# Optimization experiments

Hardware: AMD Instinct MI355X
Metric: run time of the kernel (lower is better)

The kernel has to match this reference:

```python
import jax, jax.numpy as jnp
import numpy as np

L = 4          # encoder layers
D = 1280       # d_model
H = 20         # heads
DH = D // H
FF = 5120
MEL = 128
S = 1500       # post-conv seq len
EPS = 1e-6


def quant_per_token(x):
    # dynamic per-token int8 quant: scale = max|x|/127
    s = jnp.max(jnp.abs(x), axis=-1, keepdims=True) / 127.0
    s = jnp.maximum(s, 1e-8)
    q = jnp.clip(jnp.round(x / s), -128, 127)
    return q, s


def w8a8_linear(qx, sx, w, b):
    # per-output-channel int8 weight quant, W8A8 GEMM, fp dequant epilogue
    ws = jnp.maximum(jnp.max(jnp.abs(w), axis=1, keepdims=True) / 127.0, 1e-8)  # [O,1]
    qw = jnp.clip(jnp.round(w / ws), -128, 127)
    y = qx @ qw.T                        # int-valued accum in fp32
    return y * sx * ws[:, 0][None, :] + b[None, :]


def rmsnorm_quant(x, w, b):
    # rms_norm_general: w * x / sqrt(E[x^2]+eps) + b, then per-token quant
    inv = jax.lax.rsqrt(jnp.mean(x * x, axis=-1, keepdims=True) + EPS)
    return quant_per_token(x * inv * w[None, :] + b[None, :])


def conv1d(x, w, b, stride, pad):
    y = jax.lax.conv_general_dilated(x, w, (stride,), [(pad, pad)],
                                     dimension_numbers=('NCW', 'OIW', 'NCW'))
    return y + b[None, :, None]


def setup_inputs() -> dict:
    key = jax.random.key(0)
    ks = jax.random.split(key, 24)
    n = lambda k, sh, sc=0.02: jax.random.normal(k, sh, jnp.float32) * sc
    return {
        'input_features': jax.random.normal(ks[0], (1, MEL, 2 * S), jnp.float32),
        'conv1_w': n(ks[1], (D, MEL, 3)), 'conv1_b': n(ks[2], (D,)),
        'conv2_w': n(ks[3], (D, D, 3)), 'conv2_b': n(ks[4], (D,)),
        'pos_emb': n(ks[5], (S, D)),
        'ln1_w': jnp.ones((L, D)), 'ln1_b': n(ks[6], (L, D)),
        'qkv_w': n(ks[7], (L, 3 * D, D)), 'qkv_b': n(ks[8], (L, 3 * D)),
        'out_w': n(ks[9], (L, D, D)), 'out_b': n(ks[10], (L, D)),
        'ln2_w': jnp.ones((L, D)), 'ln2_b': n(ks[11], (L, D)),
        'fc1_w': n(ks[12], (L, FF, D)), 'fc1_b': n(ks[13], (L, FF)),
        'fc2_w': n(ks[14], (L, D, FF)), 'fc2_b': n(ks[15], (L, D)),
        'lnf_w': jnp.ones((D,)), 'lnf_b': n(ks[16], (D,)),
    }


def reference(input_features, conv1_w, conv1_b, conv2_w, conv2_b, pos_emb,
              ln1_w, ln1_b, qkv_w, qkv_b, out_w, out_b,
              ln2_w, ln2_b, fc1_w, fc1_b, fc2_w, fc2_b, lnf_w, lnf_b):
    B = input_features.shape[0]
    h = jax.nn.gelu(conv1d(input_features, conv1_w, conv1_b, 1, 1))
    h = jax.nn.gelu(conv1d(h, conv2_w, conv2_b, 2, 1))
    h = h.transpose(0, 2, 1) + pos_emb[None]          # [B,S,D]
    h = h.reshape(B * S, D)
    scale = DH ** -0.5
    for l in range(L):
        res = h
        qx, sx = rmsnorm_quant(h, ln1_w[l], ln1_b[l])
        qkv = w8a8_linear(qx, sx, qkv_w[l], qkv_b[l])  # [B*S, 3D]
        q, k, v = jnp.split(qkv.reshape(B, S, 3, H, DH), 3, axis=2)
        q, k, v = q[:, :, 0], k[:, :, 0], v[:, :, 0]   # [B,S,H,DH]
        scores = jnp.einsum('bqhd,bkhd->bhqk', q, k) * scale
        attn = jax.nn.softmax(scores, axis=-1)
        ao = jnp.einsum('bhqk,bkhd->bqhd', attn, v).reshape(B * S, D)
        qa, sa = quant_per_token(ao)
        h = res + w8a8_linear(qa, sa, out_w[l], out_b[l])
        res = h
        qx, sx = rmsnorm_quant(h, ln2_w[l], ln2_b[l])
        f1 = w8a8_linear(qx, sx, fc1_w[l], fc1_b[l])
        qm, sm = quant_per_token(jax.nn.gelu(f1))
        h = res + w8a8_linear(qm, sm, fc2_w[l], fc2_b[l])
    h = h.reshape(B, S, D)
    # avg_pooler: AvgPool1d(kernel=2, stride=2) over time
    h = h.reshape(B, S // 2, 2, D).mean(axis=2)
    # final LayerNorm (true layernorm, fp path)
    mu = jnp.mean(h, axis=-1, keepdims=True)
    var = jnp.mean(jnp.square(h - mu), axis=-1, keepdims=True)
    h = (h - mu) * jax.lax.rsqrt(var + 1e-5) * lnf_w + lnf_b
    return h
```

## Files before the change

### kernel.cpp

```cpp
#include <hip/hip_runtime.h>
#include <stdint.h>

#define S_LEN 1500
#define D_MODEL 1280
#define N_HEAD 20
#define D_HEAD 64
#define FF_DIM 5120
#define N_LAYER 4

typedef int v4i __attribute__((ext_vector_type(4)));
typedef short v8s __attribute__((ext_vector_type(8)));
typedef float v4f __attribute__((ext_vector_type(4)));


__device__ inline float gelu_tanh(float x) {
    float x3 = x * x * x;
    return 0.5f * x * (1.0f + tanhf(0.7978845608028654f * (x + 0.044715f * x3)));
}

__device__ inline float wred_sum(float v) {
    for (int o = 32; o > 0; o >>= 1) v += __shfl_down(v, o, 64);
    return v;
}
__device__ inline float wred_max(float v) {
    for (int o = 32; o > 0; o >>= 1) v = fmaxf(v, __shfl_down(v, o, 64));
    return v;
}
__device__ inline float block_sum(float v, float* sm4) {
    v = wred_sum(v);
    int w = threadIdx.x >> 6;
    if ((threadIdx.x & 63) == 0) sm4[w] = v;
    __syncthreads();
    float r = sm4[0] + sm4[1] + sm4[2] + sm4[3];
    __syncthreads();
    return r;
}
__device__ inline float block_max(float v, float* sm4) {
    v = wred_max(v);
    int w = threadIdx.x >> 6;
    if ((threadIdx.x & 63) == 0) sm4[w] = v;
    __syncthreads();
    float r = fmaxf(fmaxf(sm4[0], sm4[1]), fmaxf(sm4[2], sm4[3]));
    __syncthreads();
    return r;
}

__device__ inline unsigned short f2bf(float x) {
    unsigned int u = __float_as_uint(x);
    u += 0x7fffu + ((u >> 16) & 1u);
    return (unsigned short)(u >> 16);
}
__device__ inline float bf2f(unsigned short h) {
    return __uint_as_float(((unsigned int)h) << 16);
}

__device__ inline void gload_lds16(const void* g, void* l) {
    __builtin_amdgcn_global_load_lds(
        (const __attribute__((address_space(1))) char*)g,
        (__attribute__((address_space(3))) char*)l, 16, 0, 0);
}


__global__ __launch_bounds__(256) void im2col1_kernel(
    const float* __restrict__ x, unsigned short* __restrict__ Ah,
    unsigned short* __restrict__ Al)
{
    int t = blockIdx.x * 256 + threadIdx.x;
    int col = blockIdx.y;
    if (t >= 3000) return;
    int tap = col >> 7, i = col & 127;
    int src = t - 1 + tap;
    float v = (src >= 0 && src < 3000) ? x[(size_t)i * 3000 + src] : 0.0f;
    unsigned short h = f2bf(v);
    Ah[(size_t)t * 384 + col] = h;
    Al[(size_t)t * 384 + col] = f2bf(v - bf2f(h));
}

__global__ __launch_bounds__(256) void im2col2_kernel(
    const float* __restrict__ g1, unsigned short* __restrict__ Ah,
    unsigned short* __restrict__ Al)
{
    int col = blockIdx.x * 256 + threadIdx.x;
    int t = blockIdx.y;
    if (col >= 3840) return;
    int tap = col / 1280, o = col - tap * 1280;
    int src = 2 * t - 1 + tap;
    float v = (src >= 0 && src < 3000) ? g1[(size_t)src * 1280 + o] : 0.0f;
    unsigned short h = f2bf(v);
    Ah[(size_t)t * 3840 + col] = h;
    Al[(size_t)t * 3840 + col] = f2bf(v - bf2f(h));
}

__global__ __launch_bounds__(256) void wreorder_kernel(
    const float* __restrict__ w, unsigned short* __restrict__ woh,
    unsigned short* __restrict__ wol, int C)
{
    int o = blockIdx.x;
    int KC = 3 * C;
    const float* wr = w + (size_t)o * KC;
    for (int col = threadIdx.x; col < KC; col += 256) {
        int tap = col / C, i = col - tap * C;
        float v = wr[i * 3 + tap];
        unsigned short h = f2bf(v);
        woh[(size_t)o * KC + col] = h;
        wol[(size_t)o * KC + col] = f2bf(v - bf2f(h));
    }
}

template <int EPI>
__global__ __launch_bounds__(256, 2) void gemm_conv_bf16x3(
    const unsigned short* __restrict__ Ah, const unsigned short* __restrict__ Al,
    const unsigned short* __restrict__ Wh, const unsigned short* __restrict__ Wl,
    const float* __restrict__ bias, const float* __restrict__ pos,
    float* __restrict__ out, int M, int N, int K, int nTilesN)
{
    __shared__ unsigned short lds[2][4][128][32];
    int tid = threadIdx.x;
    int lane = tid & 63;
    int wv = tid >> 6;
    int l15 = lane & 15, quad = lane >> 4;
    int wm = wv >> 1, wn = wv & 1;

    int nwg = gridDim.x;
    int cpx = nwg >> 3;
    int bid = blockIdx.x;
    int swz = (bid & 7) * cpx + (bid >> 3);
    int bx = swz % nTilesN, by = swz / nTilesN;
    int m0 = by * 128, n0 = bx * 128;

    const unsigned short* splane = (wv == 0) ? Ah : (wv == 1) ? Al : (wv == 2) ? Wh : Wl;
    int rbase = (wv < 2) ? m0 : n0;
    int rlim  = (wv < 2) ? M : N;
    const unsigned short* srcp[8];
    #pragma unroll
    for (int c = 0; c < 8; c++) {
        int row = rbase + c * 16 + (lane >> 2);
        if (row >= rlim) row = rlim - 1;
        srcp[c] = splane + (size_t)row * K + (lane & 3) * 8;
    }

    auto stage = [&](int nb, int k0) {
        char* lbase = (char*)&lds[nb][wv][0][0];
        #pragma unroll
        for (int c = 0; c < 8; c++)
            gload_lds16(srcp[c] + k0, lbase + c * 1024);
    };

    v4f acc[4][4];
    #pragma unroll
    for (int i = 0; i < 4; i++)
        #pragma unroll
        for (int j = 0; j < 4; j++) acc[i][j] = (v4f){0.0f, 0.0f, 0.0f, 0.0f};

    int nsteps = K >> 5;
    stage(0, 0);
    __syncthreads();
    int cur = 0;
    for (int t = 0; t < nsteps; t++) {
        if (t + 1 < nsteps) stage(cur ^ 1, (t + 1) * 32);
        v8s ah[4], al2[4], bh[4], bl[4];
        #pragma unroll
        for (int i = 0; i < 4; i++) {
            ah[i]  = *(const v8s*)&lds[cur][0][wm * 64 + i * 16 + l15][quad * 8];
            al2[i] = *(const v8s*)&lds[cur][1][wm * 64 + i * 16 + l15][quad * 8];
            bh[i]  = *(const v8s*)&lds[cur][2][wn * 64 + i * 16 + l15][quad * 8];
            bl[i]  = *(const v8s*)&lds[cur][3][wn * 64 + i * 16 + l15][quad * 8];
        }
        #pragma unroll
        for (int i = 0; i < 4; i++)
            #pragma unroll
            for (int j = 0; j < 4; j++) {
                acc[i][j] = __builtin_amdgcn_mfma_f32_16x16x32_bf16(ah[i],  bh[j], acc[i][j], 0, 0, 0);
                acc[i][j] = __builtin_amdgcn_mfma_f32_16x16x32_bf16(al2[i], bh[j], acc[i][j], 0, 0, 0);
                acc[i][j] = __builtin_amdgcn_mfma_f32_16x16x32_bf16(ah[i],  bl[j], acc[i][j], 0, 0, 0);
            }
        __syncthreads();
        cur ^= 1;
    }

    #pragma unroll
    for (int i = 0; i < 4; i++) {
        #pragma unroll
        for (int j = 0; j < 4; j++) {
            int n = n0 + wn * 64 + j * 16 + l15;
            float bn = bias[n];
            #pragma unroll
            for (int r = 0; r < 4; r++) {
                int m = m0 + wm * 64 + i * 16 + quad * 4 + r;
                if (m < M) {
                    float v = gelu_tanh(acc[i][j][r] + bn);
                    if (EPI == 1) v += pos[(size_t)m * N + n];
                    out[(size_t)m * N + n] = v;
                }
            }
        }
    }
}


__global__ __launch_bounds__(256) void wquant_kernel(
    const float* __restrict__ w, int8_t* __restrict__ qw,
    float* __restrict__ ws, int K)
{
    int r = blockIdx.x;
    int tid = threadIdx.x;
    __shared__ float sm4[4];
    const float4* wr = (const float4*)(w + (size_t)r * K);
    int n4 = K >> 2;
    float mx = 0.0f;
    for (int i = tid; i < n4; i += 256) {
        float4 v = wr[i];
        mx = fmaxf(mx, fmaxf(fmaxf(fabsf(v.x), fabsf(v.y)), fmaxf(fabsf(v.z), fabsf(v.w))));
    }
    mx = block_max(mx, sm4);
    float sc = fmaxf(mx / 127.0f, 1e-8f);
    if (tid == 0) ws[r] = sc;
    float rs = 1.0f / sc;
    char4* qr = (char4*)(qw + (size_t)r * K);
    for (int i = tid; i < n4; i += 256) {
        float4 v = wr[i];
        char4 q;
        q.x = (int8_t)fminf(fmaxf(rintf(v.x * rs), -128.0f), 127.0f);
        q.y = (int8_t)fminf(fmaxf(rintf(v.y * rs), -128.0f), 127.0f);
        q.z = (int8_t)fminf(fmaxf(rintf(v.z * rs), -128.0f), 127.0f);
        q.w = (int8_t)fminf(fmaxf(rintf(v.w * rs), -128.0f), 127.0f);
        qr[i] = q;
    }
}

__global__ __launch_bounds__(256) void rmsnorm_quant_kernel(
    const float* __restrict__ x, const float* __restrict__ w,
    const float* __restrict__ b, int8_t* __restrict__ q,
    float* __restrict__ sx)
{
    int s = blockIdx.x;
    int tid = threadIdx.x;
    __shared__ float sm4[4];
    const float* xr = x + (size_t)s * D_MODEL;
    float v[5];
    float ss = 0.0f;
    for (int i = 0; i < 5; i++) {
        float t = xr[tid + 256 * i];
        v[i] = t;
        ss += t * t;
    }
    ss = block_sum(ss, sm4);
    float inv = rsqrtf(ss * (1.0f / 1280.0f) + 1e-6f);
    float mx = 0.0f;
    for (int i = 0; i < 5; i++) {
        int idx = tid + 256 * i;
        float t = v[i] * inv * w[idx] + b[idx];
        v[i] = t;
        mx = fmaxf(mx, fabsf(t));
    }
    mx = block_max(mx, sm4);
    float sc = fmaxf(mx / 127.0f, 1e-8f);
    if (tid == 0) sx[s] = sc;
    float rs = 1.0f / sc;
    for (int i = 0; i < 5; i++) {
        float qv = rintf(v[i] * rs);
        qv = fminf(fmaxf(qv, -128.0f), 127.0f);
        q[(size_t)s * D_MODEL + tid + 256 * i] = (int8_t)qv;
    }
}

template <bool GELU>
__global__ __launch_bounds__(256) void quant_kernel(
    const float* __restrict__ x, int8_t* __restrict__ q,
    float* __restrict__ sx, int Dm)
{
    int s = blockIdx.x;
    int tid = threadIdx.x;
    __shared__ float sm4[4];
    const float4* xr = (const float4*)(x + (size_t)s * Dm);
    int n4 = Dm >> 2;
    float mx = 0.0f;
    for (int i = tid; i < n4; i += 256) {
        float4 t = xr[i];
        if (GELU) { t.x = gelu_tanh(t.x); t.y = gelu_tanh(t.y); t.z = gelu_tanh(t.z); t.w = gelu_tanh(t.w); }
        mx = fmaxf(mx, fmaxf(fmaxf(fabsf(t.x), fabsf(t.y)), fmaxf(fabsf(t.z), fabsf(t.w))));
    }
    mx = block_max(mx, sm4);
    float sc = fmaxf(mx / 127.0f, 1e-8f);
    if (tid == 0) sx[s] = sc;
    float rs = 1.0f / sc;
    char4* qr = (char4*)(q + (size_t)s * Dm);
    for (int i = tid; i < n4; i += 256) {
        float4 t = xr[i];
        if (GELU) { t.x = gelu_tanh(t.x); t.y = gelu_tanh(t.y); t.z = gelu_tanh(t.z); t.w = gelu_tanh(t.w); }
        char4 qq;
        qq.x = (int8_t)fminf(fmaxf(rintf(t.x * rs), -128.0f), 127.0f);
        qq.y = (int8_t)fminf(fmaxf(rintf(t.y * rs), -128.0f), 127.0f);
        qq.z = (int8_t)fminf(fmaxf(rintf(t.z * rs), -128.0f), 127.0f);
        qq.w = (int8_t)fminf(fmaxf(rintf(t.w * rs), -128.0f), 127.0f);
        qr[i] = qq;
    }
}

__global__ __launch_bounds__(256) void gemm_w8a8_mfma(
    const int8_t* __restrict__ qx, const float* __restrict__ sx,
    const int8_t* __restrict__ qw, const float* __restrict__ ws,
    const float* __restrict__ bias, const float* __restrict__ res,
    float* __restrict__ out, int M, int O, int K)
{
    int lane = threadIdx.x & 63;
    int wv = threadIdx.x >> 6;
    int l15 = lane & 15;
    int quad = lane >> 4;
    int m_base = blockIdx.y * 64 + wv * 16;
    int n_base = blockIdx.x * 64;

    int ar = m_base + l15; if (ar >= M) ar = M - 1;
    const int8_t* ap = qx + (size_t)ar * K + quad * 16;
    const int8_t* bp = qw + (size_t)(n_base + l15) * K + quad * 16;
    size_t rowK16 = (size_t)16 * K;

    v4i acc0 = {0, 0, 0, 0}, acc1 = {0, 0, 0, 0}, acc2 = {0, 0, 0, 0}, acc3 = {0, 0, 0, 0};
    int nsteps = K >> 6;
    for (int s = 0; s < nsteps; s++) {
        v4i a  = *(const v4i*)(ap + s * 64);
        v4i b0 = *(const v4i*)(bp + s * 64);
        v4i b1 = *(const v4i*)(bp + rowK16 + s * 64);
        v4i b2 = *(const v4i*)(bp + 2 * rowK16 + s * 64);
        v4i b3 = *(const v4i*)(bp + 3 * rowK16 + s * 64);
        acc0 = __builtin_amdgcn_mfma_i32_16x16x64_i8(a, b0, acc0, 0, 0, 0);
        acc1 = __builtin_amdgcn_mfma_i32_16x16x64_i8(a, b1, acc1, 0, 0, 0);
        acc2 = __builtin_amdgcn_mfma_i32_16x16x64_i8(a, b2, acc2, 0, 0, 0);
        acc3 = __builtin_amdgcn_mfma_i32_16x16x64_i8(a, b3, acc3, 0, 0, 0);
    }

    float sxv[4];
    #pragma unroll
    for (int r = 0; r < 4; r++) {
        int m = m_base + quad * 4 + r;
        sxv[r] = (m < M) ? sx[m] : 0.0f;
    }
    v4i accs[4] = {acc0, acc1, acc2, acc3};
    #pragma unroll
    for (int nb = 0; nb < 4; nb++) {
        int n = n_base + nb * 16 + l15;
        float wn = ws[n];
        float bn = bias[n];
        #pragma unroll
        for (int r = 0; r < 4; r++) {
            int m = m_base + quad * 4 + r;
            if (m < M) {
                float y = (float)accs[nb][r] * sxv[r] * wn + bn;
                if (res) y += res[(size_t)m * O + n];
                out[(size_t)m * O + n] = y;
            }
        }
    }
}

__global__ __launch_bounds__(256) void attn_tiled_kernel(
    const float* __restrict__ qkv, float* __restrict__ ao)
{
    __shared__ float Qs[64][68];
    __shared__ float KV[64][68];
    __shared__ float Ps[64][68];
    int h = blockIdx.y;
    int q_tile = blockIdx.x;
    int tid = threadIdx.x;
    int tx = tid & 15, ty = tid >> 4;
    int q0 = ty * 4;
    int d0 = tx * 4;

    {
        int r = tid >> 2;
        int dq = (tid & 3) * 16;
        int qg = q_tile * 64 + r;
        int qc = qg < S_LEN ? qg : S_LEN - 1;
        const float4* src = (const float4*)(qkv + (size_t)qc * 3840 + h * 64 + dq);
        #pragma unroll
        for (int i = 0; i < 4; i++)
            *(float4*)&Qs[r][dq + i * 4] = src[i];
    }

    float O[4][4] = {};
    float m_run[4], l_run[4];
    #pragma unroll
    for (int i = 0; i < 4; i++) { m_run[i] = -INFINITY; l_run[i] = 0.0f; }

    for (int kt = 0; kt < 24; kt++) {
        int kbase = kt * 64;
        int krem = S_LEN - kbase;

        __syncthreads();
        {
            int kk = tid >> 2;
            int dq = (tid & 3) * 16;
            int kg = kbase + kk;
            int kc = kg < S_LEN ? kg : S_LEN - 1;
            const float4* src = (const float4*)(qkv + (size_t)kc * 3840 + 1280 + h * 64 + dq);
            #pragma unroll
            for (int i = 0; i < 4; i++) {
                float4 v = src[i];
                KV[dq + i * 4 + 0][kk] = v.x;
                KV[dq + i * 4 + 1][kk] = v.y;
                KV[dq + i * 4 + 2][kk] = v.z;
                KV[dq + i * 4 + 3][kk] = v.w;
            }
        }
        __syncthreads();

        float s[4][4] = {};
        int k0loc = tx * 4;
        for (int d = 0; d < 64; d += 4) {
            float4 qv[4], kv[4];
            #pragma unroll
            for (int i = 0; i < 4; i++) qv[i] = *(const float4*)&Qs[q0 + i][d];
            #pragma unroll
            for (int dd = 0; dd < 4; dd++) kv[dd] = *(const float4*)&KV[d + dd][k0loc];
            #pragma unroll
            for (int i = 0; i < 4; i++) {
                float qa[4] = {qv[i].x, qv[i].y, qv[i].z, qv[i].w};
                #pragma unroll
                for (int dd = 0; dd < 4; dd++) {
                    float kb[4] = {kv[dd].x, kv[dd].y, kv[dd].z, kv[dd].w};
                    #pragma unroll
                    for (int j = 0; j < 4; j++)
                        s[i][j] += qa[dd] * kb[j];
                }
            }
        }

        #pragma unroll
        for (int i = 0; i < 4; i++)
            #pragma unroll
            for (int j = 0; j < 4; j++) {
                s[i][j] *= 0.125f;
                if (k0loc + j >= krem) s[i][j] = -INFINITY;
            }

        #pragma unroll
        for (int i = 0; i < 4; i++) {
            float t = fmaxf(fmaxf(s[i][0], s[i][1]), fmaxf(s[i][2], s[i][3]));
            #pragma unroll
            for (int msk = 1; msk < 16; msk <<= 1)
                t = fmaxf(t, __shfl_xor(t, msk, 64));
            float mn = fmaxf(m_run[i], t);
            float alpha = __expf(m_run[i] - mn);
            m_run[i] = mn;
            float rs = 0.0f;
            #pragma unroll
            for (int j = 0; j < 4; j++) {
                float p = __expf(s[i][j] - mn);
                s[i][j] = p;
                rs += p;
            }
            #pragma unroll
            for (int msk = 1; msk < 16; msk <<= 1)
                rs += __shfl_xor(rs, msk, 64);
            l_run[i] = l_run[i] * alpha + rs;
            #pragma unroll
            for (int j = 0; j < 4; j++) O[i][j] *= alpha;
            *(float4*)&Ps[q0 + i][k0loc] = *(float4*)&s[i][0];
        }
        __syncthreads();

        {
            int kk = tid >> 2;
            int dq = (tid & 3) * 16;
            int kg = kbase + kk;
            int kc = kg < S_LEN ? kg : S_LEN - 1;
            const float4* src = (const float4*)(qkv + (size_t)kc * 3840 + 2560 + h * 64 + dq);
            #pragma unroll
            for (int i = 0; i < 4; i++)
                *(float4*)&KV[kk][dq + i * 4] = src[i];
        }
        __syncthreads();

        for (int kb = 0; kb < 64; kb += 4) {
            float4 pv[4], vv[4];
            #pragma unroll
            for (int i = 0; i < 4; i++) pv[i] = *(const float4*)&Ps[q0 + i][kb];
            #pragma unroll
            for (int kk = 0; kk < 4; kk++) vv[kk] = *(const float4*)&KV[kb + kk][d0];
            #pragma unroll
            for (int i = 0; i < 4; i++) {
                float pa[4] = {pv[i].x, pv[i].y, pv[i].z, pv[i].w};
                #pragma unroll
                for (int kk = 0; kk < 4; kk++) {
                    float vb[4] = {vv[kk].x, vv[kk].y, vv[kk].z, vv[kk].w};
                    #pragma unroll
                    for (int j = 0; j < 4; j++)
                        O[i][j] += pa[kk] * vb[j];
                }
            }
        }
    }

    #pragma unroll
    for (int i = 0; i < 4; i++) {
        int qg = q_tile * 64 + q0 + i;
        if (qg < S_LEN) {
            float rl = 1.0f / l_run[i];
            float4 o;
            o.x = O[i][0] * rl; o.y = O[i][1] * rl; o.z = O[i][2] * rl; o.w = O[i][3] * rl;
            *(float4*)(ao + (size_t)qg * D_MODEL + h * 64 + d0) = o;
        }
    }
}

__global__ __launch_bounds__(256) void pool_ln_kernel(
    const float* __restrict__ h, const float* __restrict__ w,
    const float* __restrict__ b, float* __restrict__ out)
{
    int t = blockIdx.x;
    int tid = threadIdx.x;
    __shared__ float sm4[4];
    const float* r0 = h + (size_t)(2 * t) * D_MODEL;
    const float* r1 = r0 + D_MODEL;
    float v[5];
    float s1 = 0.0f;
    for (int i = 0; i < 5; i++) {
        int idx = tid + 256 * i;
        float x = 0.5f * (r0[idx] + r1[idx]);
        v[i] = x;
        s1 += x;
    }
    float mu = block_sum(s1, sm4) * (1.0f / 1280.0f);
    float s2 = 0.0f;
    for (int i = 0; i < 5; i++) {
        float d = v[i] - mu;
        s2 += d * d;
    }
    float var = block_sum(s2, sm4) * (1.0f / 1280.0f);
    float inv = rsqrtf(var + 1e-5f);
    for (int i = 0; i < 5; i++) {
        int idx = tid + 256 * i;
        out[(size_t)t * D_MODEL + idx] = (v[i] - mu) * inv * w[idx] + b[idx];
    }
}


static inline size_t al256(size_t x) { return (x + 255) & ~(size_t)255; }

extern "C" void kernel_launch(void* const* d_in, const int* in_sizes, int n_in,
                              void* d_out, int out_size, void* d_ws, size_t ws_size,
                              hipStream_t stream) {
    const float* in_feat = (const float*)d_in[0];
    const float* conv1_w = (const float*)d_in[1];
    const float* conv1_b = (const float*)d_in[2];
    const float* conv2_w = (const float*)d_in[3];
    const float* conv2_b = (const float*)d_in[4];
    const float* pos_emb = (const float*)d_in[5];
    const float* ln1_w   = (const float*)d_in[6];
    const float* ln1_b   = (const float*)d_in[7];
    const float* qkv_w   = (const float*)d_in[8];
    const float* qkv_b   = (const float*)d_in[9];
    const float* out_w   = (const float*)d_in[10];
    const float* out_b   = (const float*)d_in[11];
    const float* ln2_w   = (const float*)d_in[12];
    const float* ln2_b   = (const float*)d_in[13];
    const float* fc1_w   = (const float*)d_in[14];
    const float* fc1_b   = (const float*)d_in[15];
    const float* fc2_w   = (const float*)d_in[16];
    const float* fc2_b   = (const float*)d_in[17];
    const float* lnf_w   = (const float*)d_in[18];
    const float* lnf_b   = (const float*)d_in[19];
    float* outp = (float*)d_out;

    char* ws = (char*)d_ws;
    size_t off = 0;
    auto carve = [&](size_t bytes) {
        void* p = ws + off;
        off += al256(bytes);
        return p;
    };
    float*  hA      = (float*)carve((size_t)S_LEN * D_MODEL * 4);
    float*  hB      = (float*)carve((size_t)S_LEN * D_MODEL * 4);
    float*  qkvbuf  = (float*)carve((size_t)S_LEN * 3840 * 4);
    float*  aobuf   = (float*)carve((size_t)S_LEN * D_MODEL * 4);
    float*  f1buf   = (float*)carve((size_t)S_LEN * FF_DIM * 4);
    int8_t* q8      = (int8_t*)carve((size_t)S_LEN * FF_DIM);
    float*  sx      = (float*)carve((size_t)S_LEN * 4);
    int8_t* qw_qkv  = (int8_t*)carve((size_t)3840 * 1280);
    float*  ws_qkv  = (float*)carve((size_t)3840 * 4);
    int8_t* qw_out  = (int8_t*)carve((size_t)1280 * 1280);
    float*  ws_out  = (float*)carve((size_t)1280 * 4);
    int8_t* qw_fc1  = (int8_t*)carve((size_t)5120 * 1280);
    float*  ws_fc1  = (float*)carve((size_t)5120 * 4);
    int8_t* qw_fc2  = (int8_t*)carve((size_t)1280 * 5120);
    float*  ws_fc2  = (float*)carve((size_t)1280 * 4);
    (void)ws_size; (void)n_in; (void)in_sizes; (void)out_size;

    unsigned short* A1h = (unsigned short*)q8;
    unsigned short* A1l = A1h + (size_t)3000 * 384;
    unsigned short* W1h = (unsigned short*)aobuf;
    unsigned short* W1l = W1h + (size_t)1280 * 384;
    float* g1 = qkvbuf;
    unsigned short* A2h = (unsigned short*)f1buf;
    unsigned short* A2l = A2h + (size_t)1500 * 3840;
    unsigned short* W2h = (unsigned short*)qkvbuf;
    unsigned short* W2l = W2h + (size_t)1280 * 3840;

    im2col1_kernel<<<dim3(12, 384), 256, 0, stream>>>(in_feat, A1h, A1l);
    wreorder_kernel<<<1280, 256, 0, stream>>>(conv1_w, W1h, W1l, 128);
    gemm_conv_bf16x3<0><<<240, 256, 0, stream>>>(A1h, A1l, W1h, W1l, conv1_b, nullptr, g1, 3000, 1280, 384, 10);
    im2col2_kernel<<<dim3(15, 1500), 256, 0, stream>>>(g1, A2h, A2l);
    wreorder_kernel<<<1280, 256, 0, stream>>>(conv2_w, W2h, W2l, 1280);
    gemm_conv_bf16x3<1><<<120, 256, 0, stream>>>(A2h, A2l, W2h, W2l, conv2_b, pos_emb, hA, 1500, 1280, 3840, 10);

    float* h = hA;
    float* hn = hB;
    const int mtiles = (S_LEN + 63) / 64;

    for (int l = 0; l < N_LAYER; l++) {
        wquant_kernel<<<3840, 256, 0, stream>>>(qkv_w + (size_t)l * 3840 * 1280, qw_qkv, ws_qkv, 1280);
        wquant_kernel<<<1280, 256, 0, stream>>>(out_w + (size_t)l * 1280 * 1280, qw_out, ws_out, 1280);
        wquant_kernel<<<5120, 256, 0, stream>>>(fc1_w + (size_t)l * 5120 * 1280, qw_fc1, ws_fc1, 1280);
        wquant_kernel<<<1280, 256, 0, stream>>>(fc2_w + (size_t)l * 1280 * 5120, qw_fc2, ws_fc2, 5120);

        rmsnorm_quant_kernel<<<S_LEN, 256, 0, stream>>>(h, ln1_w + l * D_MODEL, ln1_b + l * D_MODEL, q8, sx);
        gemm_w8a8_mfma<<<dim3(60, mtiles), 256, 0, stream>>>(q8, sx, qw_qkv, ws_qkv,
            qkv_b + (size_t)l * 3840, nullptr, qkvbuf, S_LEN, 3840, 1280);
        attn_tiled_kernel<<<dim3(24, N_HEAD), 256, 0, stream>>>(qkvbuf, aobuf);
        quant_kernel<false><<<S_LEN, 256, 0, stream>>>(aobuf, q8, sx, D_MODEL);
        gemm_w8a8_mfma<<<dim3(20, mtiles), 256, 0, stream>>>(q8, sx, qw_out, ws_out,
            out_b + (size_t)l * 1280, h, hn, S_LEN, 1280, 1280);
        { float* t = h; h = hn; hn = t; }

        rmsnorm_quant_kernel<<<S_LEN, 256, 0, stream>>>(h, ln2_w + l * D_MODEL, ln2_b + l * D_MODEL, q8, sx);
        gemm_w8a8_mfma<<<dim3(80, mtiles), 256, 0, stream>>>(q8, sx, qw_fc1, ws_fc1,
            fc1_b + (size_t)l * 5120, nullptr, f1buf, S_LEN, 5120, 1280);
        quant_kernel<true><<<S_LEN, 256, 0, stream>>>(f1buf, q8, sx, FF_DIM);
        gemm_w8a8_mfma<<<dim3(20, mtiles), 256, 0, stream>>>(q8, sx, qw_fc2, ws_fc2,
            fc2_b + (size_t)l * 1280, h, hn, S_LEN, 1280, 5120);
        { float* t = h; h = hn; hn = t; }
    }

    pool_ln_kernel<<<750, 256, 0, stream>>>(h, lnf_w, lnf_b, outp);
}
```

Measured before the change: 2.632 ms.

## Rewrite attention with bf16x3 split MFMA instead of scalar FP32 FMA

Replaces the scalar FP32 flash-attention kernel with one that splits Q, K, V and P into bf16 high and low parts and computes QK^T and PV using three 16x16x32 bf16 MFMA products. Each wave owns 16 query rows. K and V are converted to split bf16 tiles in shared memory, and V is stored transposed for the PV operand. The goal is to move the attention FLOPs onto matrix cores while keeping near-FP32 accuracy, at the cost of conversion work, triple MFMA count and scalar, uncoalesced output stores.

Result: faster. 2.283 ms (-13.2%).

```diff
diff --git a/kernel.cpp b/kernel.cpp
--- a/kernel.cpp
+++ b/kernel.cpp
@@ -10,7 +10,9 @@
 
 typedef int v4i __attribute__((ext_vector_type(4)));
 typedef short v8s __attribute__((ext_vector_type(8)));
+typedef short v4s __attribute__((ext_vector_type(4)));
 typedef float v4f __attribute__((ext_vector_type(4)));
+typedef unsigned short ushort_t;
 
 
 __device__ inline float gelu_tanh(float x) {
@@ -353,152 +355,180 @@
     }
 }
 
-__global__ __launch_bounds__(256) void attn_tiled_kernel(
+__global__ __launch_bounds__(256, 2) void attn_mfma_kernel(
     const float* __restrict__ qkv, float* __restrict__ ao)
 {
-    __shared__ float Qs[64][68];
-    __shared__ float KV[64][68];
-    __shared__ float Ps[64][68];
+    __shared__ ushort_t Kh[64][72], Kl[64][72];
+    __shared__ ushort_t Vh[64][72], Vl[64][72];
+    __shared__ ushort_t Ph[64][72], Pl[64][72];
     int h = blockIdx.y;
     int q_tile = blockIdx.x;
     int tid = threadIdx.x;
-    int tx = tid & 15, ty = tid >> 4;
-    int q0 = ty * 4;
-    int d0 = tx * 4;
-
-    {
-        int r = tid >> 2;
-        int dq = (tid & 3) * 16;
-        int qg = q_tile * 64 + r;
-        int qc = qg < S_LEN ? qg : S_LEN - 1;
-        const float4* src = (const float4*)(qkv + (size_t)qc * 3840 + h * 64 + dq);
-        #pragma unroll
-        for (int i = 0; i < 4; i++)
-            *(float4*)&Qs[r][dq + i * 4] = src[i];
-    }
-
-    float O[4][4] = {};
+    int lane = tid & 63;
+    int wv = tid >> 6;
+    int l15 = lane & 15, quad = lane >> 4;
+
+    int qg = q_tile * 64 + wv * 16 + l15;
+    int qc = qg < S_LEN ? qg : S_LEN - 1;
+    const float* qsrc = qkv + (size_t)qc * 3840 + h * 64;
+    v8s qh[2], ql[2];
+    #pragma unroll
+    for (int ks = 0; ks < 2; ks++) {
+        const float4* p4 = (const float4*)(qsrc + ks * 32 + quad * 8);
+        float4 a = p4[0], b = p4[1];
+        float f[8] = {a.x, a.y, a.z, a.w, b.x, b.y, b.z, b.w};
+        #pragma unroll
+        for (int j = 0; j < 8; j++) {
+            unsigned short hh = f2bf(f[j]);
+            qh[ks][j] = (short)hh;
+            ql[ks][j] = (short)f2bf(f[j] - bf2f(hh));
+        }
+    }
+
+    v4f O[4];
+    #pragma unroll
+    for (int nb = 0; nb < 4; nb++) O[nb] = (v4f){0.0f, 0.0f, 0.0f, 0.0f};
     float m_run[4], l_run[4];
     #pragma unroll
-    for (int i = 0; i < 4; i++) { m_run[i] = -INFINITY; l_run[i] = 0.0f; }
+    for (int r = 0; r < 4; r++) { m_run[r] = -INFINITY; l_run[r] = 0.0f; }
+
+    int sk = tid >> 2, sd = (tid & 3) * 16;
+    int vk = (tid & 15) * 4, vd = (tid >> 4) * 4;
 
     for (int kt = 0; kt < 24; kt++) {
         int kbase = kt * 64;
         int krem = S_LEN - kbase;
 
         __syncthreads();
+
         {
-            int kk = tid >> 2;
-            int dq = (tid & 3) * 16;
-            int kg = kbase + kk;
-            int kc = kg < S_LEN ? kg : S_LEN - 1;
-            const float4* src = (const float4*)(qkv + (size_t)kc * 3840 + 1280 + h * 64 + dq);
+            int kg2 = kbase + sk;
+            int kc2 = kg2 < S_LEN ? kg2 : S_LEN - 1;
+            const float* src = qkv + (size_t)kc2 * 3840 + 1280 + h * 64 + sd;
+            float f[16];
+            *(float4*)&f[0]  = ((const float4*)src)[0];
+            *(float4*)&f[4]  = ((const float4*)src)[1];
+            *(float4*)&f[8]  = ((const float4*)src)[2];
+            *(float4*)&f[12] = ((const float4*)src)[3];
+            v8s h0, h1, l0, l1;
+            #pragma unroll
+            for (int j = 0; j < 8; j++) {
+                unsigned short u0 = f2bf(f[j]);
+                unsigned short u1 = f2bf(f[8 + j]);
+                h0[j] = (short)u0; l0[j] = (short)f2bf(f[j] - bf2f(u0));
+                h1[j] = (short)u1; l1[j] = (short)f2bf(f[8 + j] - bf2f(u1));
+            }
+            *(v8s*)&Kh[sk][sd] = h0; *(v8s*)&Kh[sk][sd + 8] = h1;
+            *(v8s*)&Kl[sk][sd] = l0; *(v8s*)&Kl[sk][sd + 8] = l1;
+        }
+        {
+            float vals[4][4];
             #pragma unroll
             for (int i = 0; i < 4; i++) {
-                float4 v = src[i];
-                KV[dq + i * 4 + 0][kk] = v.x;
-                KV[dq + i * 4 + 1][kk] = v.y;
-                KV[dq + i * 4 + 2][kk] = v.z;
-                KV[dq + i * 4 + 3][kk] = v.w;
+                int kg2 = kbase + vk + i;
+                int kc2 = kg2 < S_LEN ? kg2 : S_LEN - 1;
+                *(float4*)&vals[i][0] =
+                    *(const float4*)(qkv + (size_t)kc2 * 3840 + 2560 + h * 64 + vd);
+            }
+            #pragma unroll
+            for (int j = 0; j < 4; j++) {
+                v4s hv, lv;
+                #pragma unroll
+                for (int i = 0; i < 4; i++) {
+                    unsigned short u = f2bf(vals[i][j]);
+                    hv[i] = (short)u;
+                    lv[i] = (short)f2bf(vals[i][j] - bf2f(u));
+                }
+                *(v4s*)&Vh[vd + j][vk] = hv;
+                *(v4s*)&Vl[vd + j][vk] = lv;
             }
         }
         __syncthreads();
 
-        float s[4][4] = {};
-        int k0loc = tx * 4;
-        for (int d = 0; d < 64; d += 4) {
-            float4 qv[4], kv[4];
-            #pragma unroll
-            for (int i = 0; i < 4; i++) qv[i] = *(const float4*)&Qs[q0 + i][d];
-            #pragma unroll
-            for (int dd = 0; dd < 4; dd++) kv[dd] = *(const float4*)&KV[d + dd][k0loc];
-            #pragma unroll
-            for (int i = 0; i < 4; i++) {
-                float qa[4] = {qv[i].x, qv[i].y, qv[i].z, qv[i].w};
-                #pragma unroll
-                for (int dd = 0; dd < 4; dd++) {
-                    float kb[4] = {kv[dd].x, kv[dd].y, kv[dd].z, kv[dd].w};
-                    #pragma unroll
-                    for (int j = 0; j < 4; j++)
-                        s[i][j] += qa[dd] * kb[j];
-                }
-            }
-        }
-
-        #pragma unroll
-        for (int i = 0; i < 4; i++)
-            #pragma unroll
-            for (int j = 0; j < 4; j++) {
-                s[i][j] *= 0.125f;
-                if (k0loc + j >= krem) s[i][j] = -INFINITY;
-            }
-
-        #pragma unroll
-        for (int i = 0; i < 4; i++) {
-            float t = fmaxf(fmaxf(s[i][0], s[i][1]), fmaxf(s[i][2], s[i][3]));
+        v4f S[4];
+        #pragma unroll
+        for (int nb = 0; nb < 4; nb++) S[nb] = (v4f){0.0f, 0.0f, 0.0f, 0.0f};
+        #pragma unroll
+        for (int ks = 0; ks < 2; ks++) {
+            #pragma unroll
+            for (int nb = 0; nb < 4; nb++) {
+                v8s kbh = *(const v8s*)&Kh[nb * 16 + l15][ks * 32 + quad * 8];
+                v8s kbl = *(const v8s*)&Kl[nb * 16 + l15][ks * 32 + quad * 8];
+                S[nb] = __builtin_amdgcn_mfma_f32_16x16x32_bf16(qh[ks], kbh, S[nb], 0, 0, 0);
+                S[nb] = __builtin_amdgcn_mfma_f32_16x16x32_bf16(ql[ks], kbh, S[nb], 0, 0, 0);
+                S[nb] = __builtin_amdgcn_mfma_f32_16x16x32_bf16(qh[ks], kbl, S[nb], 0, 0, 0);
+            }
+        }
+
+        #pragma unroll
+        for (int nb = 0; nb < 4; nb++) {
+            bool valid = (nb * 16 + l15) < krem;
+            #pragma unroll
+            for (int r = 0; r < 4; r++) {
+                float s = S[nb][r] * 0.125f;
+                S[nb][r] = valid ? s : -INFINITY;
+            }
+        }
+
+        #pragma unroll
+        for (int r = 0; r < 4; r++) {
+            float t = fmaxf(fmaxf(S[0][r], S[1][r]), fmaxf(S[2][r], S[3][r]));
             #pragma unroll
             for (int msk = 1; msk < 16; msk <<= 1)
                 t = fmaxf(t, __shfl_xor(t, msk, 64));
-            float mn = fmaxf(m_run[i], t);
-            float alpha = __expf(m_run[i] - mn);
-            m_run[i] = mn;
+            float mn = fmaxf(m_run[r], t);
+            float alpha = __expf(m_run[r] - mn);
+            m_run[r] = mn;
             float rs = 0.0f;
             #pragma unroll
-            for (int j = 0; j < 4; j++) {
-                float p = __expf(s[i][j] - mn);
-                s[i][j] = p;
+            for (int nb = 0; nb < 4; nb++) {
+                float p = __expf(S[nb][r] - mn);
+                S[nb][r] = p;
                 rs += p;
             }
             #pragma unroll
             for (int msk = 1; msk < 16; msk <<= 1)
                 rs += __shfl_xor(rs, msk, 64);
-            l_run[i] = l_run[i] * alpha + rs;
-            #pragma unroll
-            for (int j = 0; j < 4; j++) O[i][j] *= alpha;
-            *(float4*)&Ps[q0 + i][k0loc] = *(float4*)&s[i][0];
+            l_run[r] = l_run[r] * alpha + rs;
+            #pragma unroll
+            for (int nb = 0; nb < 4; nb++) O[nb][r] *= alpha;
+        }
+
+        #pragma unroll
+        for (int nb = 0; nb < 4; nb++) {
+            #pragma unroll
+            for (int r = 0; r < 4; r++) {
+                float p = S[nb][r];
+                unsigned short hp = f2bf(p);
+                Ph[wv * 16 + quad * 4 + r][nb * 16 + l15] = hp;
+                Pl[wv * 16 + quad * 4 + r][nb * 16 + l15] = f2bf(p - bf2f(hp));
+            }
         }
         __syncthreads();
 
-        {
-            int kk = tid >> 2;
-            int dq = (tid & 3) * 16;
-            int kg = kbase + kk;
-            int kc = kg < S_LEN ? kg : S_LEN - 1;
-            const float4* src = (const float4*)(qkv + (size_t)kc * 3840 + 2560 + h * 64 + dq);
-            #pragma unroll
-            for (int i = 0; i < 4; i++)
-                *(float4*)&KV[kk][dq + i * 4] = src[i];
-        }
-        __syncthreads();
-
-        for (int kb = 0; kb < 64; kb += 4) {
-            float4 pv[4], vv[4];
-            #pragma unroll
-            for (int i = 0; i < 4; i++) pv[i] = *(const float4*)&Ps[q0 + i][kb];
-            #pragma unroll
-            for (int kk = 0; kk < 4; kk++) vv[kk] = *(const float4*)&KV[kb + kk][d0];
-            #pragma unroll
-            for (int i = 0; i < 4; i++) {
-                float pa[4] = {pv[i].x, pv[i].y, pv[i].z, pv[i].w};
-                #pragma unroll
-                for (int kk = 0; kk < 4; kk++) {
-                    float vb[4] = {vv[kk].x, vv[kk].y, vv[kk].z, vv[kk].w};
-                    #pragma unroll
-                    for (int j = 0; j < 4; j++)
-                        O[i][j] += pa[kk] * vb[j];
-                }
-            }
-        }
-    }
-
-    #pragma unroll
-    for (int i = 0; i < 4; i++) {
-        int qg = q_tile * 64 + q0 + i;
-        if (qg < S_LEN) {
-            float rl = 1.0f / l_run[i];
-            float4 o;
-            o.x = O[i][0] * rl; o.y = O[i][1] * rl; o.z = O[i][2] * rl; o.w = O[i][3] * rl;
-            *(float4*)(ao + (size_t)qg * D_MODEL + h * 64 + d0) = o;
+        #pragma unroll
+        for (int ks = 0; ks < 2; ks++) {
+            v8s pah = *(const v8s*)&Ph[wv * 16 + l15][ks * 32 + quad * 8];
+            v8s pal = *(const v8s*)&Pl[wv * 16 + l15][ks * 32 + quad * 8];
+            #pragma unroll
+            for (int nb = 0; nb < 4; nb++) {
+                v8s vbh = *(const v8s*)&Vh[nb * 16 + l15][ks * 32 + quad * 8];
+                v8s vbl = *(const v8s*)&Vl[nb * 16 + l15][ks * 32 + quad * 8];
+                O[nb] = __builtin_amdgcn_mfma_f32_16x16x32_bf16(pah, vbh, O[nb], 0, 0, 0);
+                O[nb] = __builtin_amdgcn_mfma_f32_16x16x32_bf16(pal, vbh, O[nb], 0, 0, 0);
+                O[nb] = __builtin_amdgcn_mfma_f32_16x16x32_bf16(pah, vbl, O[nb], 0, 0, 0);
+            }
+        }
+    }
+
+    #pragma unroll
+    for (int r = 0; r < 4; r++) {
+        int qg2 = q_tile * 64 + wv * 16 + quad * 4 + r;
+        if (qg2 < S_LEN) {
+            float rl = 1.0f / l_run[r];
+            #pragma unroll
+            for (int nb = 0; nb < 4; nb++)
+                ao[(size_t)qg2 * D_MODEL + h * 64 + nb * 16 + l15] = O[nb][r] * rl;
         }
     }
 }
@@ -616,7 +646,7 @@
         rmsnorm_quant_kernel<<<S_LEN, 256, 0, stream>>>(h, ln1_w + l * D_MODEL, ln1_b + l * D_MODEL, q8, sx);
         gemm_w8a8_mfma<<<dim3(60, mtiles), 256, 0, stream>>>(q8, sx, qw_qkv, ws_qkv,
             qkv_b + (size_t)l * 3840, nullptr, qkvbuf, S_LEN, 3840, 1280);
-        attn_tiled_kernel<<<dim3(24, N_HEAD), 256, 0, stream>>>(qkvbuf, aobuf);
+        attn_mfma_kernel<<<dim3(24, N_HEAD), 256, 0, stream>>>(qkvbuf, aobuf);
         quant_kernel<false><<<S_LEN, 256, 0, stream>>>(aobuf, q8, sx, D_MODEL);
         gemm_w8a8_mfma<<<dim3(20, mtiles), 256, 0, stream>>>(q8, sx, qw_out, ws_out,
             out_b + (size_t)l * 1280, h, hn, S_LEN, 1280, 1280);
```
